# Kernel tuning notes

Measured on AMD Instinct MI355X. Metric: run time of the kernel, lower is better.

## Reference

```python
import jax, jax.numpy as jnp
import numpy as np

B, C, T, H, W = 8, 128, 8, 56, 56
WS = (2, 7, 7)
SHIFT = (1, 3, 3)  # window_size // 2
DEPTH = 2
HEADS = 4
HEAD_DIM = C // HEADS
N = WS[0] * WS[1] * WS[2]  # 98 tokens per window
EPS = 1e-5

def _rel_pos_index():
    g = np.meshgrid(np.arange(WS[0]), np.arange(WS[1]), np.arange(WS[2]), indexing='ij')
    coords = np.stack(g).reshape(3, -1)
    rel = coords[:, :, None] - coords[:, None, :]
    rel[0] += WS[0] - 1; rel[1] += WS[1] - 1; rel[2] += WS[2] - 1
    return rel[0] * (2 * WS[1] - 1) * (2 * WS[2] - 1) + rel[1] * (2 * WS[2] - 1) + rel[2]

REL_IDX = jnp.asarray(_rel_pos_index())  # (N, N) int

def _attn_mask():
    img = np.zeros((T, H, W))
    sl = lambda w, s: (slice(0, -w), slice(-w, -s), slice(-s, None))
    cnt = 0
    for ts in sl(WS[0], SHIFT[0]):
        for hs in sl(WS[1], SHIFT[1]):
            for ws in sl(WS[2], SHIFT[2]):
                img[ts, hs, ws] = cnt; cnt += 1
    m = img.reshape(T // WS[0], WS[0], H // WS[1], WS[1], W // WS[2], WS[2])
    m = m.transpose(0, 2, 4, 1, 3, 5).reshape(-1, N)
    am = m[:, None, :] - m[:, :, None]
    return np.where(am != 0, -100.0, 0.0).astype(np.float32)

ATTN_MASK = jnp.asarray(_attn_mask())  # (nW, N, N)

def layernorm(x, g, b):
    mu = jnp.mean(x, -1, keepdims=True)
    var = jnp.var(x, -1, keepdims=True)
    return (x - mu) * jax.lax.rsqrt(var + EPS) * g + b

def window_partition(x):  # (B,T,H,W,C) -> (B*nW, N, C)
    b = x.shape[0]
    x = x.reshape(b, T // WS[0], WS[0], H // WS[1], WS[1], W // WS[2], WS[2], C)
    return x.transpose(0, 1, 3, 5, 2, 4, 6, 7).reshape(-1, N, C)

def window_reverse(w):  # (B*nW, N, C) -> (B,T,H,W,C)
    x = w.reshape(-1, T // WS[0], H // WS[1], W // WS[2], WS[0], WS[1], WS[2], C)
    return x.transpose(0, 1, 4, 2, 5, 3, 6, 7).reshape(-1, T, H, W, C)

def window_attention(xw, qkv_w, qkv_b, rpb, proj_w, proj_b, mask):
    BnW = xw.shape[0]
    qkv = (xw @ qkv_w + qkv_b).reshape(BnW, N, 3, HEADS, HEAD_DIM)
    q, k, v = qkv[:, :, 0], qkv[:, :, 1], qkv[:, :, 2]
    attn = jnp.einsum('wnhd,wmhd->whnm', q * HEAD_DIM ** -0.5, k)
    attn = attn + rpb[REL_IDX].transpose(2, 0, 1)[None]  # (1,h,N,N) relative position bias
    if mask is not None:
        nW = mask.shape[0]
        attn = (attn.reshape(BnW // nW, nW, HEADS, N, N) + mask[None, :, None]).reshape(BnW, HEADS, N, N)
    attn = jax.nn.softmax(attn, axis=-1)
    out = jnp.einsum('whnm,wmhd->wnhd', attn, v).reshape(BnW, N, C)
    return out @ proj_w + proj_b

def _forward(x, ln1_g, ln1_b, qkv_w, qkv_b, rpb, proj_w, proj_b, ln2_g, ln2_b, fc1_w, fc1_b, fc2_w, fc2_b):
    x = x.transpose(0, 2, 3, 4, 1)  # (B,T,H,W,C)
    for i in range(DEPTH):
        shifted = (i % 2 == 1)
        y = layernorm(x, ln1_g[i], ln1_b[i])
        if shifted:
            y = jnp.roll(y, (-SHIFT[0], -SHIFT[1], -SHIFT[2]), axis=(1, 2, 3))
        yw = window_attention(window_partition(y), qkv_w[i], qkv_b[i], rpb[i],
                              proj_w[i], proj_b[i], ATTN_MASK if shifted else None)
        y = window_reverse(yw)
        if shifted:
            y = jnp.roll(y, SHIFT, axis=(1, 2, 3))
        x = x + y  # residual (drop_path=0, eval mode)
        h = layernorm(x, ln2_g[i], ln2_b[i])
        h = jax.nn.gelu(h @ fc1_w[i] + fc1_b[i], approximate=False) @ fc2_w[i] + fc2_b[i]
        x = x + h
    return x.transpose(0, 4, 1, 2, 3)  # (B,C,T,H,W)

def setup_inputs():
    key = jax.random.key(0)
    ks = jax.random.split(key, 6)
    D4 = 4 * C
    RPB = (2 * WS[0] - 1) * (2 * WS[1] - 1) * (2 * WS[2] - 1)  # 507
    return {
        'x': jax.random.normal(ks[0], (B, C, T, H, W), jnp.float32),
        'ln1_g': jnp.ones((DEPTH, C), jnp.float32),
        'ln1_b': jnp.zeros((DEPTH, C), jnp.float32),
        'qkv_w': jax.random.normal(ks[1], (DEPTH, C, 3 * C), jnp.float32) * 0.02,
        'qkv_b': jnp.zeros((DEPTH, 3 * C), jnp.float32),
        'rpb': jax.random.normal(ks[2], (DEPTH, RPB, HEADS), jnp.float32) * 0.02,
        'proj_w': jax.random.normal(ks[3], (DEPTH, C, C), jnp.float32) * 0.02,
        'proj_b': jnp.zeros((DEPTH, C), jnp.float32),
        'ln2_g': jnp.ones((DEPTH, C), jnp.float32),
        'ln2_b': jnp.zeros((DEPTH, C), jnp.float32),
        'fc1_w': jax.random.normal(ks[4], (DEPTH, C, D4), jnp.float32) * 0.02,
        'fc1_b': jnp.zeros((DEPTH, D4), jnp.float32),
        'fc2_w': jax.random.normal(ks[5], (DEPTH, D4, C), jnp.float32) * 0.02,
        'fc2_b': jnp.zeros((DEPTH, C), jnp.float32),
    }

def reference(x, ln1_g, ln1_b, qkv_w, qkv_b, rpb, proj_w, proj_b, ln2_g, ln2_b, fc1_w, fc1_b, fc2_w, fc2_b):
    return _forward(x, ln1_g, ln1_b, qkv_w, qkv_b, rpb, proj_w, proj_b, ln2_g, ln2_b, fc1_w, fc1_b, fc2_w, fc2_b)
```

## Files before the change

kernel.cpp:

```cpp
#include <hip/hip_runtime.h>
#include <hip/hip_bf16.h>

typedef __attribute__((ext_vector_type(8))) short sv8_t;
typedef __attribute__((ext_vector_type(4))) float fv4_t;
typedef __attribute__((ext_vector_type(4))) float f4ld_t;

#define BB 8
#define TT 8
#define HH 56
#define WW2 56
#define NTOK 98
#define BNW 2048
#define PSPAT 25088
#define TOK_TOTAL 200704
#define ACT_ELEMS 25690112
#define VT_WSTRIDE 14336

#define SWZB(row, cb) ((cb) ^ ((((unsigned)(row)) & 7u) << 4))

__device__ __forceinline__ unsigned short f2bf(float f) {
    union { float f; unsigned u; } x; x.f = f;
    unsigned r = x.u + 0x7fffu + ((x.u >> 16) & 1u);
    return (unsigned short)(r >> 16);
}
__device__ __forceinline__ unsigned packbf(float lo, float hi) {
    __hip_bfloat162 h = __float22bfloat162_rn(make_float2(lo, hi));
    union { __hip_bfloat162 h; unsigned u; } cv; cv.h = h; return cv.u;
}
__device__ __forceinline__ sv8_t lds_ld8(const unsigned short* p, int byteoff) {
    return *(const sv8_t*)((const char*)p + byteoff);
}
__device__ __forceinline__ void lds_st8(unsigned short* p, int byteoff, sv8_t v) {
    *(sv8_t*)((char*)p + byteoff) = v;
}
__device__ __forceinline__ void lds_st1(unsigned short* p, int byteoff, unsigned short v) {
    *(unsigned short*)((char*)p + byteoff) = v;
}
__device__ __forceinline__ float gelu_f(float v) {
    float e = __expf(-1.702f * v);
    return v * __builtin_amdgcn_rcpf(1.f + e);
}

__global__ __launch_bounds__(256) void k_transpose_in(const float* __restrict__ in,
                                                      float* __restrict__ xbuf) {
    __shared__ float tile[32][33];
    int p0 = blockIdx.x * 32, c0 = blockIdx.y * 32, b = blockIdx.z;
    int pi = threadIdx.x, ci = threadIdx.y;
    const float* src = in + ((size_t)b * 128 + c0) * PSPAT + p0;
    for (int r = 0; r < 32; r += 8)
        tile[ci + r][pi] = src[(size_t)(ci + r) * PSPAT + pi];
    __syncthreads();
    float* dst = xbuf + ((size_t)b * PSPAT + p0) * 128 + c0;
    for (int r = 0; r < 32; r += 8)
        dst[(size_t)(ci + r) * 128 + pi] = tile[pi][ci + r];
}

__global__ __launch_bounds__(256) void k_prep_w(const float* __restrict__ in,
                                                unsigned short* __restrict__ out,
                                                int K, int N) {
    __shared__ float tile[32][33];
    int n0 = blockIdx.x * 32, k0 = blockIdx.y * 32;
    int x = threadIdx.x, y = threadIdx.y;
    for (int r = 0; r < 32; r += 8)
        tile[y + r][x] = in[(size_t)(k0 + y + r) * N + n0 + x];
    __syncthreads();
    for (int r = 0; r < 32; r += 8)
        out[(size_t)(n0 + y + r) * K + k0 + x] = f2bf(tile[x][y + r]);
}

__global__ void k_prep_bias(const float* __restrict__ rpb, float* __restrict__ biasb) {
    int col = threadIdx.x;
    int row = blockIdx.x;
    int head = blockIdx.y;
    int layer = blockIdx.z;
    int tn = min(row, 97), tm = min(col, 97);
    int itn = tn / 49, rn = tn - itn * 49, ihn = rn / 7, iwn = rn - ihn * 7;
    int itm = tm / 49, rm = tm - itm * 49, ihm = rm / 7, iwm = rm - ihm * 7;
    int dt = itn - itm + 1, dh = ihn - ihm + 6, dw = iwn - iwm + 6;
    float v = rpb[((size_t)layer * 507 + dt * 169 + dh * 13 + dw) * 4 + head];
    biasb[(((size_t)layer * 4 + head) * 112 + row) * 112 + col] = v;
}

__global__ __launch_bounds__(256) void k_qkv(const float* __restrict__ xbuf,
                                             const float* __restrict__ g,
                                             const float* __restrict__ be,
                                             const unsigned short* __restrict__ wT,
                                             const float* __restrict__ bias,
                                             unsigned short* __restrict__ qkbuf,
                                             unsigned short* __restrict__ vT,
                                             int shifted) {
    __shared__ unsigned short xt[64 * 128];
    int tid = threadIdx.x;
    int row0 = blockIdx.x * 64;
    {
        int r = tid >> 2, q = tid & 3;
        int wt = row0 + r;
        int win = wt / 98, n = wt - win * 98;
        int b_ = win >> 8, wrem = win & 255;
        int tw = wrem >> 6, hw = (wrem >> 3) & 7, ww = wrem & 7;
        int it = n / 49, r2 = n - it * 49, ih = r2 / 7, iw = r2 - ih * 7;
        int t = tw * 2 + it, h = hw * 7 + ih, w = ww * 7 + iw;
        if (shifted) {
            t += 1; if (t >= TT) t -= TT;
            h += 3; if (h >= HH) h -= HH;
            w += 3; if (w >= WW2) w -= WW2;
        }
        const float* src = xbuf + ((size_t)b_ * PSPAT + t * (HH * WW2) + h * WW2 + w) * 128 + q * 32;
        float v[32];
        float s = 0.f, sq = 0.f;
        for (int i = 0; i < 8; i++) {
            f4ld_t f = *(const f4ld_t*)(src + i * 4);
            v[i * 4 + 0] = f.x; v[i * 4 + 1] = f.y; v[i * 4 + 2] = f.z; v[i * 4 + 3] = f.w;
            s += f.x + f.y + f.z + f.w;
            sq += f.x * f.x + f.y * f.y + f.z * f.z + f.w * f.w;
        }
        s += __shfl_xor(s, 1); sq += __shfl_xor(sq, 1);
        s += __shfl_xor(s, 2); sq += __shfl_xor(sq, 2);
        float mu = s * (1.f / 128.f);
        float var = sq * (1.f / 128.f) - mu * mu;
        float rs = rsqrtf(var + 1e-5f);
        for (int c0 = 0; c0 < 32; c0 += 8) {
            float y[8];
            #pragma unroll
            for (int i = 0; i < 8; i++) {
                int c = q * 32 + c0 + i;
                y[i] = (v[c0 + i] - mu) * rs * g[c] + be[c];
            }
            union { unsigned u[4]; sv8_t s8; } pk;
            pk.u[0] = packbf(y[0], y[1]); pk.u[1] = packbf(y[2], y[3]);
            pk.u[2] = packbf(y[4], y[5]); pk.u[3] = packbf(y[6], y[7]);
            lds_st8(xt, r * 256 + SWZB(r, (q * 32 + c0) * 2), pk.s8);
        }
    }
    __syncthreads();
    int wv = tid >> 6, lane = tid & 63, l15 = lane & 15, lhi = lane >> 4;

    if (wv < 2) {
        int nb = wv * 128;
        fv4_t acc[4][8];
        for (int m = 0; m < 4; m++) for (int f = 0; f < 8; f++) acc[m][f] = (fv4_t){0.f, 0.f, 0.f, 0.f};
        for (int kk = 0; kk < 4; kk++) {
            sv8_t x4[4];
            #pragma unroll
            for (int m = 0; m < 4; m++) {
                int ar = 16 * m + l15;
                x4[m] = lds_ld8(xt, ar * 256 + SWZB(ar, (kk * 32 + 8 * lhi) * 2));
            }
            #pragma unroll
            for (int f = 0; f < 8; f++) {
                sv8_t wf = *(const sv8_t*)(wT + (size_t)(nb + 16 * f + l15) * 128 + kk * 32 + 8 * lhi);
                #pragma unroll
                for (int m = 0; m < 4; m++)
                    acc[m][f] = __builtin_amdgcn_mfma_f32_16x16x32_bf16(wf, x4[m], acc[m][f], 0, 0, 0);
            }
        }
        float sc_ = (wv == 0) ? 0.17677669529663687f : 1.f;
        #pragma unroll
        for (int f = 0; f < 8; f++) {
            f4ld_t b4 = *(const f4ld_t*)(bias + nb + 16 * f + 4 * lhi);
            #pragma unroll
            for (int m = 0; m < 4; m++) {
                int row = row0 + 16 * m + l15;
                union { unsigned u[2]; uint2 u2; } pk;
                pk.u[0] = packbf((acc[m][f][0] + b4.x) * sc_, (acc[m][f][1] + b4.y) * sc_);
                pk.u[1] = packbf((acc[m][f][2] + b4.z) * sc_, (acc[m][f][3] + b4.w) * sc_);
                *(uint2*)(qkbuf + (size_t)row * 256 + nb + 16 * f + 4 * lhi) = pk.u2;
            }
        }
    } else {
        int d16base = (wv - 2) * 4;
        fv4_t acc[4][4];
        for (int m = 0; m < 4; m++) for (int f = 0; f < 4; f++) acc[m][f] = (fv4_t){0.f, 0.f, 0.f, 0.f};
        for (int kk = 0; kk < 4; kk++) {
            sv8_t x4[4];
            #pragma unroll
            for (int m = 0; m < 4; m++) {
                int ar = 16 * m + l15;
                x4[m] = lds_ld8(xt, ar * 256 + SWZB(ar, (kk * 32 + 8 * lhi) * 2));
            }
            #pragma unroll
            for (int f = 0; f < 4; f++) {
                sv8_t wf = *(const sv8_t*)(wT + (size_t)(256 + (d16base + f) * 16 + l15) * 128 + kk * 32 + 8 * lhi);
                #pragma unroll
                for (int m = 0; m < 4; m++)
                    acc[m][f] = __builtin_amdgcn_mfma_f32_16x16x32_bf16(wf, x4[m], acc[m][f], 0, 0, 0);
            }
        }
        #pragma unroll
        for (int f = 0; f < 4; f++) {
            f4ld_t b4 = *(const f4ld_t*)(bias + 256 + (d16base + f) * 16 + 4 * lhi);
            #pragma unroll
            for (int r = 0; r < 4; r++) {
                int d = (d16base + f) * 16 + 4 * lhi + r;
                #pragma unroll
                for (int m = 0; m < 4; m++) {
                    int row = row0 + 16 * m + l15;
                    int win = row / 98, tok = row - win * 98;
                    vT[(size_t)win * VT_WSTRIDE + d * 112 + tok] = f2bf(acc[m][f][r] + b4[r]);
                }
            }
        }
    }
}

__global__ __launch_bounds__(256, 3) void k_attn_proj(const unsigned short* __restrict__ qk,
                                                      const unsigned short* __restrict__ vT,
                                                      const float* __restrict__ biasb,
                                                      const unsigned short* __restrict__ pwT,
                                                      const float* __restrict__ pb,
                                                      float* __restrict__ xbuf,
                                                      int shifted) {
    __shared__ unsigned short ot[112 * 128];
    __shared__ int lablut[112];
    int win = blockIdx.x;
    int tid = threadIdx.x;
    int wv = tid >> 6, lane = tid & 63;
    int head = wv;
    int l15 = lane & 15, lhi = lane >> 4;
    int wrem = win & 255;
    int tw = wrem >> 6, hw = (wrem >> 3) & 7, ww = wrem & 7;

    for (int m = tid; m < 112; m += 256) {
        int t0 = min(m, 97);
        int it = t0 / 49, r2 = t0 - it * 49, ih = r2 / 7, iw = r2 - ih * 7;
        int lab = 0;
        if (shifted) {
            int t = tw * 2 + it, h = hw * 7 + ih, w = ww * 7 + iw;
            int ct = (t < TT - 2) ? 0 : ((t < TT - 1) ? 1 : 2);
            int ch = (h < HH - 7) ? 0 : ((h < HH - 3) ? 1 : 2);
            int cw = (w < WW2 - 7) ? 0 : ((w < WW2 - 3) ? 1 : 2);
            lab = ct * 9 + ch * 3 + cw;
        }
        lablut[m] = lab;
    }
    __syncthreads();

    size_t rowbase = (size_t)win * 98;
    sv8_t kf[7];
    #pragma unroll
    for (int j = 0; j < 7; j++) {
        int tok = min(16 * j + l15, 97);
        kf[j] = *(const sv8_t*)(qk + (rowbase + tok) * 256 + 128 + head * 32 + 8 * lhi);
    }
    const unsigned short* vbase = vT + (size_t)win * VT_WSTRIDE + (head * 32) * 112;
    sv8_t vf[4][2];
    #pragma unroll
    for (int kk = 0; kk < 4; kk++)
        #pragma unroll
        for (int j = 0; j < 2; j++)
            vf[kk][j] = *(const sv8_t*)(vbase + (16 * j + l15) * 112 + kk * 32 + 8 * lhi);

    int klab[7];
    if (shifted) {
        #pragma unroll
        for (int j = 0; j < 7; j++) {
            int kb = 16 * j + 4 * lhi;
            klab[j] = lablut[kb] | (lablut[kb + 1] << 8) | (lablut[kb + 2] << 16) | (lablut[kb + 3] << 24);
        }
    }

    int src0 = ((lane & 16) << 1) + l15;
    int src1 = src0 + 16;
    bool jlo = (lane < 32);

    sv8_t qa_c = *(const sv8_t*)(qk + (rowbase + l15) * 256 + head * 32 + 8 * lhi);

    for (int ms = 0; ms < 7; ms++) {
        sv8_t qa_n = qa_c;
        if (ms < 6) {
            int qtok = min(16 * (ms + 1) + l15, 97);
            qa_n = *(const sv8_t*)(qk + (rowbase + qtok) * 256 + head * 32 + 8 * lhi);
        }
        int ql = min(16 * ms + l15, 97);
        int labq = shifted ? lablut[ql] : 0;
        const float* bq = biasb + ((size_t)head * 112 + ql) * 112;
        f4ld_t bv[7];
        #pragma unroll
        for (int j = 0; j < 7; j++)
            bv[j] = *(const f4ld_t*)(bq + 16 * j + 4 * lhi);
        fv4_t sc[7];
        __builtin_amdgcn_s_setprio(1);
        #pragma unroll
        for (int j = 0; j < 7; j++) {
            fv4_t z = {0.f, 0.f, 0.f, 0.f};
            sc[j] = __builtin_amdgcn_mfma_f32_16x16x32_bf16(kf[j], qa_c, z, 0, 0, 0);
        }
        __builtin_amdgcn_s_setprio(0);
        float mx = -1e30f;
        #pragma unroll
        for (int j = 0; j < 7; j++) {
            #pragma unroll
            for (int r = 0; r < 4; r++) {
                float s = sc[j][r] + bv[j][r];
                if (shifted && (((klab[j] >> (8 * r)) & 255) != labq)) s -= 100.f;
                if (16 * j + 4 * lhi + r >= 98) s = -1e30f;
                sc[j][r] = s;
                mx = fmaxf(mx, s);
            }
        }
        mx = fmaxf(mx, __shfl_xor(mx, 16));
        mx = fmaxf(mx, __shfl_xor(mx, 32));
        float sm = 0.f;
        #pragma unroll
        for (int j = 0; j < 7; j++)
            #pragma unroll
            for (int r = 0; r < 4; r++) {
                float p = __expf(sc[j][r] - mx);
                sc[j][r] = p;
                sm += p;
            }
        sm += __shfl_xor(sm, 16);
        sm += __shfl_xor(sm, 32);
        float inv = __builtin_amdgcn_rcpf(sm);
        int pkl[8], pkh[8];
        #pragma unroll
        for (int j = 0; j < 7; j++) {
            pkl[j] = (int)packbf(sc[j][0] * inv, sc[j][1] * inv);
            pkh[j] = (int)packbf(sc[j][2] * inv, sc[j][3] * inv);
        }
        pkl[7] = 0; pkh[7] = 0;
        fv4_t oacc[2] = {{0.f, 0.f, 0.f, 0.f}, {0.f, 0.f, 0.f, 0.f}};
        #pragma unroll
        for (int kk = 0; kk < 4; kk++) {
            int e_lo0 = __shfl(pkl[2 * kk], src0), o_lo0 = __shfl(pkl[2 * kk + 1], src0);
            int e_hi0 = __shfl(pkh[2 * kk], src0), o_hi0 = __shfl(pkh[2 * kk + 1], src0);
            int e_lo1 = __shfl(pkl[2 * kk], src1), o_lo1 = __shfl(pkl[2 * kk + 1], src1);
            int e_hi1 = __shfl(pkh[2 * kk], src1), o_hi1 = __shfl(pkh[2 * kk + 1], src1);
            union { int u[4]; sv8_t s8; } pa;
            pa.u[0] = jlo ? e_lo0 : o_lo0;
            pa.u[1] = jlo ? e_hi0 : o_hi0;
            pa.u[2] = jlo ? e_lo1 : o_lo1;
            pa.u[3] = jlo ? e_hi1 : o_hi1;
            __builtin_amdgcn_s_setprio(1);
            #pragma unroll
            for (int j = 0; j < 2; j++)
                oacc[j] = __builtin_amdgcn_mfma_f32_16x16x32_bf16(pa.s8, vf[kk][j], oacc[j], 0, 0, 0);
            __builtin_amdgcn_s_setprio(0);
        }
        #pragma unroll
        for (int r = 0; r < 4; r++) {
            int orow = 16 * ms + 4 * lhi + r;
            #pragma unroll
            for (int j = 0; j < 2; j++) {
                int ocol = head * 32 + 16 * j + l15;
                float v = (orow < 98) ? oacc[j][r] : 0.f;
                lds_st1(ot, orow * 256 + SWZB(orow, ocol * 2), f2bf(v));
            }
        }
        qa_c = qa_n;
    }
    __syncthreads();

    {
        int nb = wv * 32;
        fv4_t acc[7][2];
        for (int m = 0; m < 7; m++) for (int j = 0; j < 2; j++) acc[m][j] = (fv4_t){0.f, 0.f, 0.f, 0.f};
        for (int kk = 0; kk < 4; kk++) {
            sv8_t b[2];
            #pragma unroll
            for (int j = 0; j < 2; j++)
                b[j] = *(const sv8_t*)(pwT + (size_t)(nb + 16 * j + l15) * 128 + kk * 32 + 8 * lhi);
            __builtin_amdgcn_s_setprio(1);
            #pragma unroll
            for (int m = 0; m < 7; m++) {
                int ar = 16 * m + l15;
                sv8_t a = lds_ld8(ot, ar * 256 + SWZB(ar, (kk * 32 + 8 * lhi) * 2));
                #pragma unroll
                for (int j = 0; j < 2; j++)
                    acc[m][j] = __builtin_amdgcn_mfma_f32_16x16x32_bf16(a, b[j], acc[m][j], 0, 0, 0);
            }
            __builtin_amdgcn_s_setprio(0);
        }
        int b_ = win >> 8;
        for (int m = 0; m < 7; m++)
            #pragma unroll
            for (int r = 0; r < 4; r++) {
                int row = 16 * m + lhi * 4 + r;
                if (row < 98) {
                    int it = row / 49, r2 = row - it * 49, ih = r2 / 7, iw = r2 - ih * 7;
                    int t = tw * 2 + it, h = hw * 7 + ih, w = ww * 7 + iw;
                    if (shifted) {
                        t += 1; if (t >= TT) t -= TT;
                        h += 3; if (h >= HH) h -= HH;
                        w += 3; if (w >= WW2) w -= WW2;
                    }
                    float* xp = xbuf + ((size_t)b_ * PSPAT + t * (HH * WW2) + h * WW2 + w) * 128 + nb;
                    #pragma unroll
                    for (int j = 0; j < 2; j++) {
                        int c = 16 * j + l15;
                        xp[c] += acc[m][j][r] + pb[nb + c];
                    }
                }
            }
    }
}

#define LOAD_CHUNK(c, R)                                                                   \
    if ((c) < 16) {                                                                        \
        if (((c) & 2) == 0) {                                                              \
            _Pragma("unroll")                                                              \
            for (int i_ = 0; i_ < 4; i_++)                                                 \
                R[i_] = *(const sv8_t*)(w1T + (size_t)(((c) >> 2) * 128 + ((c)&1) * 64 + i_ * 16 + r1) * 128 + (c1 >> 1)); \
        } else {                                                                           \
            _Pragma("unroll")                                                              \
            for (int i_ = 0; i_ < 4; i_++)                                                 \
                R[i_] = *(const sv8_t*)(w2T + (size_t)(i_ * 32 + r2) * 512 + ((c) >> 2) * 128 + ((c)&1) * 64 + (c2 >> 1)); \
        }                                                                                  \
    }
#define WRITE_CHUNK(c, R)                                                                  \
    if ((c) < 16) {                                                                        \
        unsigned short* bst_ = Bst[(c)&1];                                                 \
        if (((c) & 2) == 0) {                                                              \
            _Pragma("unroll")                                                              \
            for (int i_ = 0; i_ < 4; i_++)                                                 \
                lds_st8(bst_, (i_ * 16 + r1) * 256 + SWZB(i_ * 16 + r1, c1), R[i_]);       \
        } else {                                                                           \
            _Pragma("unroll")                                                              \
            for (int i_ = 0; i_ < 4; i_++)                                                 \
                lds_st8(bst_, (i_ * 32 + r2) * 128 + SWZB(i_ * 32 + r2, c2), R[i_]);       \
        }                                                                                  \
    }

__global__ __launch_bounds__(256, 2) void k_mlp(const float* __restrict__ xin,
                                                const float* __restrict__ g,
                                                const float* __restrict__ be,
                                                const unsigned short* __restrict__ w1T,
                                                const float* __restrict__ b1p,
                                                const unsigned short* __restrict__ w2T,
                                                const float* __restrict__ b2p,
                                                float* __restrict__ xbuf,
                                                float* __restrict__ outp,
                                                int final_layer) {
    __shared__ unsigned short A[4][32 * 128];
    __shared__ unsigned short Bst[2][8192];
    int tid = threadIdx.x;
    int wv = tid >> 6, lane = tid & 63, l15 = lane & 15, lhi = lane >> 4;
    unsigned short* bw = A[wv];
    int tok0 = blockIdx.x * 128 + wv * 32;

    int r1 = tid >> 4, c1 = (tid & 15) * 16;
    int r2 = tid >> 3, c2 = (tid & 7) * 16;

    sv8_t wA[4], wB[4];
    LOAD_CHUNK(0, wA)

    #pragma unroll
    for (int tf = 0; tf < 2; tf++) {
        int lrow = 16 * tf + l15;
        const float* src = xin + (size_t)(tok0 + lrow) * 128 + lhi * 32;
        float v[32];
        float s = 0.f, sq = 0.f;
        #pragma unroll
        for (int i = 0; i < 8; i++) {
            f4ld_t f = *(const f4ld_t*)(src + i * 4);
            v[i * 4 + 0] = f.x; v[i * 4 + 1] = f.y; v[i * 4 + 2] = f.z; v[i * 4 + 3] = f.w;
            s += f.x + f.y + f.z + f.w;
            sq += f.x * f.x + f.y * f.y + f.z * f.z + f.w * f.w;
        }
        s += __shfl_xor(s, 16); sq += __shfl_xor(sq, 16);
        s += __shfl_xor(s, 32); sq += __shfl_xor(sq, 32);
        float mu = s * (1.f / 128.f);
        float var = sq * (1.f / 128.f) - mu * mu;
        float rs = rsqrtf(var + 1e-5f);
        #pragma unroll
        for (int j = 0; j < 4; j++) {
            int c0 = lhi * 32 + 8 * j;
            f4ld_t g0 = *(const f4ld_t*)(g + c0);
            f4ld_t g1 = *(const f4ld_t*)(g + c0 + 4);
            f4ld_t b0 = *(const f4ld_t*)(be + c0);
            f4ld_t b1 = *(const f4ld_t*)(be + c0 + 4);
            float y0 = (v[8 * j + 0] - mu) * rs * g0.x + b0.x;
            float y1 = (v[8 * j + 1] - mu) * rs * g0.y + b0.y;
            float y2 = (v[8 * j + 2] - mu) * rs * g0.z + b0.z;
            float y3 = (v[8 * j + 3] - mu) * rs * g0.w + b0.w;
            float y4 = (v[8 * j + 4] - mu) * rs * g1.x + b1.x;
            float y5 = (v[8 * j + 5] - mu) * rs * g1.y + b1.y;
            float y6 = (v[8 * j + 6] - mu) * rs * g1.z + b1.z;
            float y7 = (v[8 * j + 7] - mu) * rs * g1.w + b1.w;
            union { unsigned u[4]; sv8_t s8; } pk;
            pk.u[0] = packbf(y0, y1); pk.u[1] = packbf(y2, y3);
            pk.u[2] = packbf(y4, y5); pk.u[3] = packbf(y6, y7);
            lds_st8(bw, lrow * 256 + SWZB(lrow, 64 * lhi + 16 * j), pk.s8);
        }
    }
    sv8_t xf[2][4];
    #pragma unroll
    for (int tf = 0; tf < 2; tf++)
        #pragma unroll
        for (int kk = 0; kk < 4; kk++) {
            int lrow = 16 * tf + l15;
            xf[tf][kk] = lds_ld8(bw, lrow * 256 + SWZB(lrow, 64 * kk + 16 * lhi));
        }

    fv4_t acc2[8][2];
    #pragma unroll
    for (int cg = 0; cg < 8; cg++)
        #pragma unroll
        for (int tf = 0; tf < 2; tf++) acc2[cg][tf] = (fv4_t){0.f, 0.f, 0.f, 0.f};

    WRITE_CHUNK(0, wA)
    LOAD_CHUNK(1, wB)
    __syncthreads();

    #pragma unroll
    for (int q = 0; q < 4; q++) {
        {
            const int c = 4 * q;
            WRITE_CHUNK(c + 1, wB)
            LOAD_CHUNK(c + 2, wA)
            #pragma unroll
            for (int f = 0; f < 4; f++) {
                int fg = f;
                sv8_t wf[4];
                #pragma unroll
                for (int kk = 0; kk < 4; kk++) {
                    int wrow = 16 * f + l15;
                    wf[kk] = lds_ld8(Bst[0], wrow * 256 + SWZB(wrow, kk * 64 + 16 * lhi));
                }
                fv4_t a1[2] = {{0.f, 0.f, 0.f, 0.f}, {0.f, 0.f, 0.f, 0.f}};
                __builtin_amdgcn_s_setprio(1);
                #pragma unroll
                for (int kk = 0; kk < 4; kk++) {
                    a1[0] = __builtin_amdgcn_mfma_f32_16x16x32_bf16(wf[kk], xf[0][kk], a1[0], 0, 0, 0);
                    a1[1] = __builtin_amdgcn_mfma_f32_16x16x32_bf16(wf[kk], xf[1][kk], a1[1], 0, 0, 0);
                }
                __builtin_amdgcn_s_setprio(0);
                f4ld_t b4 = *(const f4ld_t*)(b1p + q * 128 + 16 * fg + 4 * lhi);
                #pragma unroll
                for (int tf = 0; tf < 2; tf++) {
                    float g0 = gelu_f(a1[tf][0] + b4.x);
                    float g1 = gelu_f(a1[tf][1] + b4.y);
                    float g2 = gelu_f(a1[tf][2] + b4.z);
                    float g3 = gelu_f(a1[tf][3] + b4.w);
                    union { unsigned u[2]; uint2 u2; } pk;
                    pk.u[0] = packbf(g0, g1); pk.u[1] = packbf(g2, g3);
                    int lrow = 16 * tf + l15;
                    *(uint2*)((char*)bw + lrow * 256 + SWZB(lrow, 32 * fg + 8 * lhi)) = pk.u2;
                }
            }
            __syncthreads();
        }
        {
            const int c = 4 * q + 1;
            WRITE_CHUNK(c + 1, wA)
            LOAD_CHUNK(c + 2, wB)
            #pragma unroll
            for (int f = 0; f < 4; f++) {
                int fg = 4 + f;
                sv8_t wf[4];
                #pragma unroll
                for (int kk = 0; kk < 4; kk++) {
                    int wrow = 16 * f + l15;
                    wf[kk] = lds_ld8(Bst[1], wrow * 256 + SWZB(wrow, kk * 64 + 16 * lhi));
                }
                fv4_t a1[2] = {{0.f, 0.f, 0.f, 0.f}, {0.f, 0.f, 0.f, 0.f}};
                __builtin_amdgcn_s_setprio(1);
                #pragma unroll
                for (int kk = 0; kk < 4; kk++) {
                    a1[0] = __builtin_amdgcn_mfma_f32_16x16x32_bf16(wf[kk], xf[0][kk], a1[0], 0, 0, 0);
                    a1[1] = __builtin_amdgcn_mfma_f32_16x16x32_bf16(wf[kk], xf[1][kk], a1[1], 0, 0, 0);
                }
                __builtin_amdgcn_s_setprio(0);
                f4ld_t b4 = *(const f4ld_t*)(b1p + q * 128 + 16 * fg + 4 * lhi);
                #pragma unroll
                for (int tf = 0; tf < 2; tf++) {
                    float g0 = gelu_f(a1[tf][0] + b4.x);
                    float g1 = gelu_f(a1[tf][1] + b4.y);
                    float g2 = gelu_f(a1[tf][2] + b4.z);
                    float g3 = gelu_f(a1[tf][3] + b4.w);
                    union { unsigned u[2]; uint2 u2; } pk;
                    pk.u[0] = packbf(g0, g1); pk.u[1] = packbf(g2, g3);
                    int lrow = 16 * tf + l15;
                    *(uint2*)((char*)bw + lrow * 256 + SWZB(lrow, 32 * fg + 8 * lhi)) = pk.u2;
                }
            }
            __syncthreads();
        }
        {
            const int c = 4 * q + 2;
            WRITE_CHUNK(c + 1, wB)
            LOAD_CHUNK(c + 2, wA)
            #pragma unroll
            for (int kq = 0; kq < 2; kq++) {
                sv8_t uf[2];
                #pragma unroll
                for (int tf = 0; tf < 2; tf++) {
                    int lrow = 16 * tf + l15;
                    uf[tf] = lds_ld8(bw, lrow * 256 + SWZB(lrow, 64 * kq + 16 * lhi));
                }
                #pragma unroll
                for (int cb = 0; cb < 2; cb++) {
                    sv8_t w2f[4];
                    #pragma unroll
                    for (int cc = 0; cc < 4; cc++) {
                        int wrow = 16 * (4 * cb + cc) + l15;
                        w2f[cc] = lds_ld8(Bst[0], wrow * 128 + SWZB(wrow, kq * 64 + 16 * lhi));
                    }
                    __builtin_amdgcn_s_setprio(1);
                    #pragma unroll
                    for (int cc = 0; cc < 4; cc++) {
                        int cg = 4 * cb + cc;
                        acc2[cg][0] = __builtin_amdgcn_mfma_f32_16x16x32_bf16(w2f[cc], uf[0], acc2[cg][0], 0, 0, 0);
                        acc2[cg][1] = __builtin_amdgcn_mfma_f32_16x16x32_bf16(w2f[cc], uf[1], acc2[cg][1], 0, 0, 0);
                    }
                    __builtin_amdgcn_s_setprio(0);
                }
            }
            __syncthreads();
        }
        {
            const int c = 4 * q + 3;
            WRITE_CHUNK(c + 1, wA)
            LOAD_CHUNK(c + 2, wB)
            #pragma unroll
            for (int kq = 2; kq < 4; kq++) {
                sv8_t uf[2];
                #pragma unroll
                for (int tf = 0; tf < 2; tf++) {
                    int lrow = 16 * tf + l15;
                    uf[tf] = lds_ld8(bw, lrow * 256 + SWZB(lrow, 64 * kq + 16 * lhi));
                }
                #pragma unroll
                for (int cb = 0; cb < 2; cb++) {
                    sv8_t w2f[4];
                    #pragma unroll
                    for (int cc = 0; cc < 4; cc++) {
                        int wrow = 16 * (4 * cb + cc) + l15;
                        w2f[cc] = lds_ld8(Bst[1], wrow * 128 + SWZB(wrow, (kq - 2) * 64 + 16 * lhi));
                    }
                    __builtin_amdgcn_s_setprio(1);
                    #pragma unroll
                    for (int cc = 0; cc < 4; cc++) {
                        int cg = 4 * cb + cc;
                        acc2[cg][0] = __builtin_amdgcn_mfma_f32_16x16x32_bf16(w2f[cc], uf[0], acc2[cg][0], 0, 0, 0);
                        acc2[cg][1] = __builtin_amdgcn_mfma_f32_16x16x32_bf16(w2f[cc], uf[1], acc2[cg][1], 0, 0, 0);
                    }
                    __builtin_amdgcn_s_setprio(0);
                }
            }
            __syncthreads();
        }
    }
    if (!final_layer) {
        #pragma unroll
        for (int tf = 0; tf < 2; tf++) {
            int row = tok0 + 16 * tf + l15;
            #pragma unroll
            for (int cg = 0; cg < 8; cg++) {
                int c0 = 16 * cg + 4 * lhi;
                f4ld_t b4 = *(const f4ld_t*)(b2p + c0);
                float* xp = xbuf + (size_t)row * 128 + c0;
                f4ld_t o = *(f4ld_t*)xp;
                o.x += acc2[cg][tf][0] + b4.x;
                o.y += acc2[cg][tf][1] + b4.y;
                o.z += acc2[cg][tf][2] + b4.z;
                o.w += acc2[cg][tf][3] + b4.w;
                *(f4ld_t*)xp = o;
            }
        }
    } else {
        #pragma unroll
        for (int tf = 0; tf < 2; tf++) {
            int row = tok0 + 16 * tf + l15;
            int b_ = row / PSPAT, p = row - b_ * PSPAT;
            float* ob = outp + (size_t)b_ * 128 * PSPAT + p;
            #pragma unroll
            for (int cg = 0; cg < 8; cg++) {
                int c0 = 16 * cg + 4 * lhi;
                f4ld_t b4 = *(const f4ld_t*)(b2p + c0);
                const float* xp = xbuf + (size_t)row * 128 + c0;
                f4ld_t o = *(const f4ld_t*)xp;
                o.x += acc2[cg][tf][0] + b4.x;
                o.y += acc2[cg][tf][1] + b4.y;
                o.z += acc2[cg][tf][2] + b4.z;
                o.w += acc2[cg][tf][3] + b4.w;
                ob[(size_t)(c0 + 0) * PSPAT] = o.x;
                ob[(size_t)(c0 + 1) * PSPAT] = o.y;
                ob[(size_t)(c0 + 2) * PSPAT] = o.z;
                ob[(size_t)(c0 + 3) * PSPAT] = o.w;
            }
        }
    }
}

extern "C" void kernel_launch(void* const* d_in, const int* in_sizes, int n_in,
                              void* d_out, int out_size, void* d_ws, size_t ws_size,
                              hipStream_t stream) {
    const float* x_in   = (const float*)d_in[0];
    const float* ln1_g  = (const float*)d_in[1];
    const float* ln1_b  = (const float*)d_in[2];
    const float* qkv_w  = (const float*)d_in[3];
    const float* qkv_b  = (const float*)d_in[4];
    const float* rpb    = (const float*)d_in[5];
    const float* proj_w = (const float*)d_in[6];
    const float* proj_b = (const float*)d_in[7];
    const float* ln2_g  = (const float*)d_in[8];
    const float* ln2_b  = (const float*)d_in[9];
    const float* fc1_w  = (const float*)d_in[10];
    const float* fc1_b  = (const float*)d_in[11];
    const float* fc2_w  = (const float*)d_in[12];
    const float* fc2_b  = (const float*)d_in[13];
    float* out = (float*)d_out;

    char* ws = (char*)d_ws;
    float* xbuf = (float*)ws;
    unsigned short* qkbuf = (unsigned short*)(ws + 102760448);
    unsigned short* vTbuf = (unsigned short*)(ws + 205520896);
    unsigned short* wbase = (unsigned short*)(ws + 264241408);
    float* biasb = (float*)(ws + 264241408 + 786432);

    k_transpose_in<<<dim3(PSPAT / 32, 4, BB), dim3(32, 8), 0, stream>>>(x_in, xbuf);

    for (int l = 0; l < 2; l++) {
        unsigned short* wqT = wbase + (size_t)l * 196608;
        unsigned short* wpT = wqT + 49152;
        unsigned short* w1T = wpT + 16384;
        unsigned short* w2T = w1T + 65536;
        k_prep_w<<<dim3(12, 4), dim3(32, 8), 0, stream>>>(qkv_w + (size_t)l * 49152, wqT, 128, 384);
        k_prep_w<<<dim3(4, 4),  dim3(32, 8), 0, stream>>>(proj_w + (size_t)l * 16384, wpT, 128, 128);
        k_prep_w<<<dim3(16, 4), dim3(32, 8), 0, stream>>>(fc1_w + (size_t)l * 65536, w1T, 128, 512);
        k_prep_w<<<dim3(4, 16), dim3(32, 8), 0, stream>>>(fc2_w + (size_t)l * 65536, w2T, 512, 128);
    }
    k_prep_bias<<<dim3(112, 4, 2), 112, 0, stream>>>(rpb, biasb);

    for (int layer = 0; layer < 2; layer++) {
        unsigned short* wqT = wbase + (size_t)layer * 196608;
        unsigned short* wpT = wqT + 49152;
        unsigned short* w1T = wpT + 16384;
        unsigned short* w2T = w1T + 65536;
        int shifted = layer & 1;

        k_qkv<<<TOK_TOTAL / 64, 256, 0, stream>>>(xbuf, ln1_g + layer * 128, ln1_b + layer * 128,
                                                  wqT, qkv_b + layer * 384, qkbuf, vTbuf, shifted);
        k_attn_proj<<<BNW, 256, 0, stream>>>(qkbuf, vTbuf, biasb + (size_t)layer * 4 * 112 * 112,
                                             wpT, proj_b + layer * 128, xbuf, shifted);
        k_mlp<<<TOK_TOTAL / 128, 256, 0, stream>>>(xbuf, ln2_g + layer * 128, ln2_b + layer * 128,
                                                   w1T, fc1_b + layer * 512, w2T, fc2_b + layer * 128,
                                                   xbuf, out, layer == 1);
    }
}
```

Before: 779.0 us.

## Interleave fc1/fc2 chunks in MLP to halve hidden LDS buffer and raise occupancy

```diff
diff --git a/kernel.cpp b/kernel.cpp
--- a/kernel.cpp
+++ b/kernel.cpp
@@ -397,20 +397,20 @@
 
 #define LOAD_CHUNK(c, R)                                                                   \
     if ((c) < 16) {                                                                        \
-        if (((c) & 2) == 0) {                                                              \
+        if (((c) & 1) == 0) {                                                              \
             _Pragma("unroll")                                                              \
             for (int i_ = 0; i_ < 4; i_++)                                                 \
-                R[i_] = *(const sv8_t*)(w1T + (size_t)(((c) >> 2) * 128 + ((c)&1) * 64 + i_ * 16 + r1) * 128 + (c1 >> 1)); \
+                R[i_] = *(const sv8_t*)(w1T + (size_t)(((c) >> 2) * 128 + (((c) >> 1) & 1) * 64 + i_ * 16 + r1) * 128 + (c1 >> 1)); \
         } else {                                                                           \
             _Pragma("unroll")                                                              \
             for (int i_ = 0; i_ < 4; i_++)                                                 \
-                R[i_] = *(const sv8_t*)(w2T + (size_t)(i_ * 32 + r2) * 512 + ((c) >> 2) * 128 + ((c)&1) * 64 + (c2 >> 1)); \
+                R[i_] = *(const sv8_t*)(w2T + (size_t)(i_ * 32 + r2) * 512 + ((c) >> 2) * 128 + (((c) >> 1) & 1) * 64 + (c2 >> 1)); \
         }                                                                                  \
     }
 #define WRITE_CHUNK(c, R)                                                                  \
     if ((c) < 16) {                                                                        \
         unsigned short* bst_ = Bst[(c)&1];                                                 \
-        if (((c) & 2) == 0) {                                                              \
+        if (((c) & 1) == 0) {                                                              \
             _Pragma("unroll")                                                              \
             for (int i_ = 0; i_ < 4; i_++)                                                 \
                 lds_st8(bst_, (i_ * 16 + r1) * 256 + SWZB(i_ * 16 + r1, c1), R[i_]);       \
@@ -421,7 +421,7 @@
         }                                                                                  \
     }
 
-__global__ __launch_bounds__(256, 2) void k_mlp(const float* __restrict__ xin,
+__global__ __launch_bounds__(256, 3) void k_mlp(const float* __restrict__ xin,
                                                 const float* __restrict__ g,
                                                 const float* __restrict__ be,
                                                 const unsigned short* __restrict__ w1T,
@@ -431,11 +431,12 @@
                                                 float* __restrict__ xbuf,
                                                 float* __restrict__ outp,
                                                 int final_layer) {
-    __shared__ unsigned short A[4][32 * 128];
+    __shared__ unsigned short A[4][32 * 64];
     __shared__ unsigned short Bst[2][8192];
     int tid = threadIdx.x;
     int wv = tid >> 6, lane = tid & 63, l15 = lane & 15, lhi = lane >> 4;
-    unsigned short* bw = A[wv];
+    unsigned short* uw = A[wv];
+    unsigned short* xts = &Bst[0][0];
     int tok0 = blockIdx.x * 128 + wv * 32;
 
     int r1 = tid >> 4, c1 = (tid & 15) * 16;
@@ -447,6 +448,7 @@
     #pragma unroll
     for (int tf = 0; tf < 2; tf++) {
         int lrow = 16 * tf + l15;
+        int grow = wv * 32 + lrow;
         const float* src = xin + (size_t)(tok0 + lrow) * 128 + lhi * 32;
         float v[32];
         float s = 0.f, sq = 0.f;
@@ -480,7 +482,7 @@
             union { unsigned u[4]; sv8_t s8; } pk;
             pk.u[0] = packbf(y0, y1); pk.u[1] = packbf(y2, y3);
             pk.u[2] = packbf(y4, y5); pk.u[3] = packbf(y6, y7);
-            lds_st8(bw, lrow * 256 + SWZB(lrow, 64 * lhi + 16 * j), pk.s8);
+            lds_st8(xts, grow * 256 + SWZB(grow, 64 * lhi + 16 * j), pk.s8);
         }
     }
     sv8_t xf[2][4];
@@ -488,8 +490,8 @@
     for (int tf = 0; tf < 2; tf++)
         #pragma unroll
         for (int kk = 0; kk < 4; kk++) {
-            int lrow = 16 * tf + l15;
-            xf[tf][kk] = lds_ld8(bw, lrow * 256 + SWZB(lrow, 64 * kk + 16 * lhi));
+            int grow = wv * 32 + 16 * tf + l15;
+            xf[tf][kk] = lds_ld8(xts, grow * 256 + SWZB(grow, 64 * kk + 16 * lhi));
         }
 
     fv4_t acc2[8][2];
@@ -498,6 +500,7 @@
         #pragma unroll
         for (int tf = 0; tf < 2; tf++) acc2[cg][tf] = (fv4_t){0.f, 0.f, 0.f, 0.f};
 
+    __syncthreads();
     WRITE_CHUNK(0, wA)
     LOAD_CHUNK(1, wB)
     __syncthreads();
@@ -510,7 +513,6 @@
             LOAD_CHUNK(c + 2, wA)
             #pragma unroll
             for (int f = 0; f < 4; f++) {
-                int fg = f;
                 sv8_t wf[4];
                 #pragma unroll
                 for (int kk = 0; kk < 4; kk++) {
@@ -525,7 +527,7 @@
                     a1[1] = __builtin_amdgcn_mfma_f32_16x16x32_bf16(wf[kk], xf[1][kk], a1[1], 0, 0, 0);
                 }
                 __builtin_amdgcn_s_setprio(0);
-                f4ld_t b4 = *(const f4ld_t*)(b1p + q * 128 + 16 * fg + 4 * lhi);
+                f4ld_t b4 = *(const f4ld_t*)(b1p + q * 128 + 16 * f + 4 * lhi);
                 #pragma unroll
                 for (int tf = 0; tf < 2; tf++) {
                     float g0 = gelu_f(a1[tf][0] + b4.x);
@@ -535,7 +537,7 @@
                     union { unsigned u[2]; uint2 u2; } pk;
                     pk.u[0] = packbf(g0, g1); pk.u[1] = packbf(g2, g3);
                     int lrow = 16 * tf + l15;
-                    *(uint2*)((char*)bw + lrow * 256 + SWZB(lrow, 32 * fg + 8 * lhi)) = pk.u2;
+                    *(uint2*)((char*)uw + lrow * 128 + SWZB(lrow, 32 * f + 8 * lhi)) = pk.u2;
                 }
             }
             __syncthreads();
@@ -545,48 +547,12 @@
             WRITE_CHUNK(c + 1, wA)
             LOAD_CHUNK(c + 2, wB)
             #pragma unroll
-            for (int f = 0; f < 4; f++) {
-                int fg = 4 + f;
-                sv8_t wf[4];
-                #pragma unroll
-                for (int kk = 0; kk < 4; kk++) {
-                    int wrow = 16 * f + l15;
-                    wf[kk] = lds_ld8(Bst[1], wrow * 256 + SWZB(wrow, kk * 64 + 16 * lhi));
-                }
-                fv4_t a1[2] = {{0.f, 0.f, 0.f, 0.f}, {0.f, 0.f, 0.f, 0.f}};
-                __builtin_amdgcn_s_setprio(1);
-                #pragma unroll
-                for (int kk = 0; kk < 4; kk++) {
-                    a1[0] = __builtin_amdgcn_mfma_f32_16x16x32_bf16(wf[kk], xf[0][kk], a1[0], 0, 0, 0);
-                    a1[1] = __builtin_amdgcn_mfma_f32_16x16x32_bf16(wf[kk], xf[1][kk], a1[1], 0, 0, 0);
-                }
-                __builtin_amdgcn_s_setprio(0);
-                f4ld_t b4 = *(const f4ld_t*)(b1p + q * 128 + 16 * fg + 4 * lhi);
-                #pragma unroll
-                for (int tf = 0; tf < 2; tf++) {
-                    float g0 = gelu_f(a1[tf][0] + b4.x);
-                    float g1 = gelu_f(a1[tf][1] + b4.y);
-                    float g2 = gelu_f(a1[tf][2] + b4.z);
-                    float g3 = gelu_f(a1[tf][3] + b4.w);
-                    union { unsigned u[2]; uint2 u2; } pk;
-                    pk.u[0] = packbf(g0, g1); pk.u[1] = packbf(g2, g3);
-                    int lrow = 16 * tf + l15;
-                    *(uint2*)((char*)bw + lrow * 256 + SWZB(lrow, 32 * fg + 8 * lhi)) = pk.u2;
-                }
-            }
-            __syncthreads();
-        }
-        {
-            const int c = 4 * q + 2;
-            WRITE_CHUNK(c + 1, wB)
-            LOAD_CHUNK(c + 2, wA)
-            #pragma unroll
-            for (int kq = 0; kq < 2; kq++) {
+            for (int kql = 0; kql < 2; kql++) {
                 sv8_t uf[2];
                 #pragma unroll
                 for (int tf = 0; tf < 2; tf++) {
                     int lrow = 16 * tf + l15;
-                    uf[tf] = lds_ld8(bw, lrow * 256 + SWZB(lrow, 64 * kq + 16 * lhi));
+                    uf[tf] = lds_ld8(uw, lrow * 128 + SWZB(lrow, 64 * kql + 16 * lhi));
                 }
                 #pragma unroll
                 for (int cb = 0; cb < 2; cb++) {
@@ -594,7 +560,7 @@
                     #pragma unroll
                     for (int cc = 0; cc < 4; cc++) {
                         int wrow = 16 * (4 * cb + cc) + l15;
-                        w2f[cc] = lds_ld8(Bst[0], wrow * 128 + SWZB(wrow, kq * 64 + 16 * lhi));
+                        w2f[cc] = lds_ld8(Bst[1], wrow * 128 + SWZB(wrow, kql * 64 + 16 * lhi));
                     }
                     __builtin_amdgcn_s_setprio(1);
                     #pragma unroll
@@ -609,16 +575,51 @@
             __syncthreads();
         }
         {
+            const int c = 4 * q + 2;
+            WRITE_CHUNK(c + 1, wB)
+            LOAD_CHUNK(c + 2, wA)
+            #pragma unroll
+            for (int f = 0; f < 4; f++) {
+                sv8_t wf[4];
+                #pragma unroll
+                for (int kk = 0; kk < 4; kk++) {
+                    int wrow = 16 * f + l15;
+                    wf[kk] = lds_ld8(Bst[0], wrow * 256 + SWZB(wrow, kk * 64 + 16 * lhi));
+                }
+                fv4_t a1[2] = {{0.f, 0.f, 0.f, 0.f}, {0.f, 0.f, 0.f, 0.f}};
+                __builtin_amdgcn_s_setprio(1);
+                #pragma unroll
+                for (int kk = 0; kk < 4; kk++) {
+                    a1[0] = __builtin_amdgcn_mfma_f32_16x16x32_bf16(wf[kk], xf[0][kk], a1[0], 0, 0, 0);
+                    a1[1] = __builtin_amdgcn_mfma_f32_16x16x32_bf16(wf[kk], xf[1][kk], a1[1], 0, 0, 0);
+                }
+                __builtin_amdgcn_s_setprio(0);
+                f4ld_t b4 = *(const f4ld_t*)(b1p + q * 128 + 64 + 16 * f + 4 * lhi);
+                #pragma unroll
+                for (int tf = 0; tf < 2; tf++) {
+                    float g0 = gelu_f(a1[tf][0] + b4.x);
+                    float g1 = gelu_f(a1[tf][1] + b4.y);
+                    float g2 = gelu_f(a1[tf][2] + b4.z);
+                    float g3 = gelu_f(a1[tf][3] + b4.w);
+                    union { unsigned u[2]; uint2 u2; } pk;
+                    pk.u[0] = packbf(g0, g1); pk.u[1] = packbf(g2, g3);
+                    int lrow = 16 * tf + l15;
+                    *(uint2*)((char*)uw + lrow * 128 + SWZB(lrow, 32 * f + 8 * lhi)) = pk.u2;
+                }
+            }
+            __syncthreads();
+        }
+        {
             const int c = 4 * q + 3;
             WRITE_CHUNK(c + 1, wA)
             LOAD_CHUNK(c + 2, wB)
             #pragma unroll
-            for (int kq = 2; kq < 4; kq++) {
+            for (int kql = 0; kql < 2; kql++) {
                 sv8_t uf[2];
                 #pragma unroll
                 for (int tf = 0; tf < 2; tf++) {
                     int lrow = 16 * tf + l15;
-                    uf[tf] = lds_ld8(bw, lrow * 256 + SWZB(lrow, 64 * kq + 16 * lhi));
+                    uf[tf] = lds_ld8(uw, lrow * 128 + SWZB(lrow, 64 * kql + 16 * lhi));
                 }
                 #pragma unroll
                 for (int cb = 0; cb < 2; cb++) {
@@ -626,7 +627,7 @@
                     #pragma unroll
                     for (int cc = 0; cc < 4; cc++) {
                         int wrow = 16 * (4 * cb + cc) + l15;
-                        w2f[cc] = lds_ld8(Bst[1], wrow * 128 + SWZB(wrow, (kq - 2) * 64 + 16 * lhi));
+                        w2f[cc] = lds_ld8(Bst[1], wrow * 128 + SWZB(wrow, kql * 64 + 16 * lhi));
                     }
                     __builtin_amdgcn_s_setprio(1);
                     #pragma unroll
```

New measurement: 774.5 us. No clear change (-0.6%).
